# Optimization experiments

Measured on AMD Instinct MI355X. Metric: run time of the kernel, lower is better.

## Reference

```python
import jax, jax.numpy as jnp
import numpy as np

B, L, D, H, FF = 2, 2048, 2048, 16, 8192
DH = D // H
NEG = -1e9


def setup_inputs() -> dict:
    key = jax.random.key(0)
    ks = jax.random.split(key, 9)
    x = jax.random.normal(ks[0], (B, L, D), dtype=jnp.float32)
    # additive causal mask, broadcastable to [B, H, L, L]
    causal = jnp.triu(jnp.full((L, L), NEG, dtype=jnp.float32), k=1)
    mask = causal[None, None, :, :]
    s = 1.0 / np.sqrt(D)
    Wq = jax.random.normal(ks[1], (D, D), dtype=jnp.float32) * s
    Wk = jax.random.normal(ks[2], (D, D), dtype=jnp.float32) * s
    Wv = jax.random.normal(ks[3], (D, D), dtype=jnp.float32) * s
    Wo = jax.random.normal(ks[4], (D, D), dtype=jnp.float32) * s
    W_up = jax.random.normal(ks[5], (FF, D), dtype=jnp.float32) * s
    b_up = jnp.zeros((FF,), dtype=jnp.float32)
    W_down = jax.random.normal(ks[6], (D, FF), dtype=jnp.float32) * (1.0 / np.sqrt(FF))
    return {"x": x, "mask": mask, "Wq": Wq, "Wk": Wk, "Wv": Wv, "Wo": Wo,
            "W_up": W_up, "b_up": b_up, "W_down": W_down}


def reference(x, mask, Wq, Wk, Wv, Wo, W_up, b_up, W_down):
    b, l, d = x.shape
    # projections (torch Linear: y = x @ W.T); reshape to [B, H, L, DH]
    q = (x @ Wq.T).reshape(b, l, H, DH).transpose(0, 2, 1, 3)
    k = (x @ Wk.T).reshape(b, l, H, DH).transpose(0, 2, 1, 3)
    v = (x @ Wv.T).reshape(b, l, H, DH).transpose(0, 2, 1, 3)
    # NOTE: original module applies NO 1/sqrt(d_head) scaling
    scores = jnp.einsum('bhqd,bhkd->bhqk', q, k) + mask
    attn = jax.nn.softmax(scores, axis=-1)
    out = jnp.einsum('bhqk,bhkd->bhqd', attn, v)
    out = out.transpose(0, 2, 1, 3).reshape(b, l, d)
    x = x + out @ Wo.T
    h = jax.nn.relu(x @ W_up.T + b_up)
    return x + h @ W_down.T
```

## Files before the change

### kernel.cpp

```cpp
#include <hip/hip_runtime.h>
#include <stdint.h>

typedef _Float16 f16;
typedef __attribute__((ext_vector_type(8))) _Float16 f16x8;
typedef __attribute__((ext_vector_type(4))) _Float16 f16x4;
typedef __attribute__((ext_vector_type(2))) __fp16 fp16x2;
typedef __attribute__((ext_vector_type(4))) float f32x4;
typedef __attribute__((ext_vector_type(16))) float f32x16;
typedef __attribute__((ext_vector_type(4))) unsigned u32x4;

__device__ __forceinline__ void gload16(void* lds, const void* gc) {
  void* g = const_cast<void*>(gc);
  __builtin_amdgcn_global_load_lds((__attribute__((address_space(1))) void*)g,
                                   (__attribute__((address_space(3))) void*)lds,
                                   16, 0, 0);
}

__device__ __forceinline__ unsigned pkrtz(float a, float b) {
  union { fp16x2 h; unsigned u; } c;
  c.h = __builtin_amdgcn_cvt_pkrtz(a, b);
  return c.u;
}

__global__ __launch_bounds__(256) void k_cast(const float* __restrict__ in,
                                              f16* __restrict__ out, int n4) {
  int stride = gridDim.x * blockDim.x;
  for (int i = blockIdx.x * blockDim.x + threadIdx.x; i < n4; i += stride) {
    float4 v = ((const float4*)in)[i];
    f16x4 o;
    o[0] = (f16)v.x; o[1] = (f16)v.y; o[2] = (f16)v.z; o[3] = (f16)v.w;
    ((f16x4*)out)[i] = o;
  }
}

__global__ __launch_bounds__(256) void k_cast4(const float* __restrict__ s0, const float* __restrict__ s1,
                                               const float* __restrict__ s2, const float* __restrict__ s3,
                                               f16* __restrict__ d0, f16* __restrict__ d1,
                                               f16* __restrict__ d2, f16* __restrict__ d3, int n4) {
  const int which = blockIdx.y;
  const float* in = which == 0 ? s0 : which == 1 ? s1 : which == 2 ? s2 : s3;
  f16* out = which == 0 ? d0 : which == 1 ? d1 : which == 2 ? d2 : d3;
  int stride = gridDim.x * blockDim.x;
  for (int i = blockIdx.x * blockDim.x + threadIdx.x; i < n4; i += stride) {
    float4 v = ((const float4*)in)[i];
    f16x4 o;
    o[0] = (f16)v.x; o[1] = (f16)v.y; o[2] = (f16)v.z; o[3] = (f16)v.w;
    ((f16x4*)out)[i] = o;
  }
}

__global__ __launch_bounds__(256) void k_cast2w(const float* __restrict__ s0, const float* __restrict__ s1,
                                                f16* __restrict__ d0, f16* __restrict__ d1, int n4) {
  const int which = blockIdx.y;
  const float* in = which == 0 ? s0 : s1;
  f16* out = which == 0 ? d0 : d1;
  int stride = gridDim.x * blockDim.x;
  for (int i = blockIdx.x * blockDim.x + threadIdx.x; i < n4; i += stride) {
    float4 v = ((const float4*)in)[i];
    f16x4 o;
    o[0] = (f16)v.x; o[1] = (f16)v.y; o[2] = (f16)v.z; o[3] = (f16)v.w;
    ((f16x4*)out)[i] = o;
  }
}

__global__ __launch_bounds__(256) void k_transpose_v(const f16* __restrict__ vp,
                                                     f16* __restrict__ vt) {
  __shared__ __attribute__((aligned(16))) f16 tile[64][66];
  const int lt = blockIdx.x, dt = blockIdx.y, bh = blockIdx.z;
  const int t = threadIdx.x;
  const int r = t >> 3, c = 8 * (t & 7);
  const f16* src = vp + ((size_t)bh * 2048 + lt * 64) * 128 + dt * 64;
#pragma unroll
  for (int i = 0; i < 2; ++i) {
    union { f16x8 v; unsigned u[4]; } uu;
    uu.v = *(const f16x8*)&src[(size_t)(i * 32 + r) * 128 + c];
#pragma unroll
    for (int j = 0; j < 4; ++j)
      *(unsigned*)&tile[i * 32 + r][c + 2 * j] = uu.u[j];
  }
  __syncthreads();
  f16* dst = vt + ((size_t)bh * 128 + dt * 64) * 2048 + lt * 64;
#pragma unroll
  for (int i = 0; i < 2; ++i) {
    const int dr = i * 32 + r;
    f16x8 o;
#pragma unroll
    for (int e = 0; e < 8; ++e) o[e] = tile[c + e][dr];
    *(f16x8*)&dst[(size_t)dr * 2048 + c] = o;
  }
}

__global__ __launch_bounds__(256) void k_fuseout(const f16* __restrict__ x1b,
                                                 const float* __restrict__ p0,
                                                 const float* __restrict__ p1,
                                                 float* __restrict__ out, int n4) {
  int stride = gridDim.x * blockDim.x;
  for (int i = blockIdx.x * blockDim.x + threadIdx.x; i < n4; i += stride) {
    float4 a = ((const float4*)p0)[i];
    float4 b = ((const float4*)p1)[i];
    f16x4 xb = ((const f16x4*)x1b)[i];
    float4 o;
    o.x = (float)xb[0] + a.x + b.x;
    o.y = (float)xb[1] + a.y + b.y;
    o.z = (float)xb[2] + a.z + b.z;
    o.w = (float)xb[3] + a.w + b.w;
    ((float4*)out)[i] = o;
  }
}

template <int EPI, int SPLITOUT, int BK>
__global__ __launch_bounds__(256, 4) void gemm_nt(const f16* __restrict__ A,
                                                  const f16* __restrict__ B,
                                                  int Kit, int ld, int N,
                                                  const float* __restrict__ res,
                                                  f16* __restrict__ outb) {
  constexpr int TSZ = 128 * BK;
  constexpr int CH  = 2048;
  constexpr int RPC = CH / BK;
  constexpr int NCH = 128 / RPC;
  constexpr int CW  = BK / 8;
  __shared__ __attribute__((aligned(16))) f16 As[TSZ];
  __shared__ __attribute__((aligned(16))) f16 Bs[TSZ];
  const int t = threadIdx.x;
  const int l = t & 63;
  const int w = t >> 6;
  const int wr = w >> 1, wc = w & 1;

  const int nwg = gridDim.x * gridDim.y;
  const int id = blockIdx.y * gridDim.x + blockIdx.x;
  const int sw = (id & 7) * (nwg >> 3) + (id >> 3);
  const int bn = sw % gridDim.x;
  const int bm = sw / gridDim.x;

  f32x4 acc[4][4] = {};

  const size_t aoff = (size_t)bm * 128 * ld;
  const size_t boff = (size_t)bn * 128 * ld;

  const int sr = t / CW;
  const int sc = 8 * (t % CW);
  const int lbase = w * 512;

  const int lr = l & 15, lq = l >> 4;
  const int nk = Kit / BK;
  for (int kt = 0; kt < nk; ++kt) {
    const size_t gbase = (size_t)kt * BK + (size_t)sr * ld + sc;
#pragma unroll
    for (int j = 0; j < NCH; ++j) {
      gload16(As + j * CH + lbase, A + aoff + (size_t)j * RPC * ld + gbase);
      gload16(Bs + j * CH + lbase, B + boff + (size_t)j * RPC * ld + gbase);
    }
    __syncthreads();
#pragma unroll
    for (int kk = 0; kk < BK / 32; ++kk) {
      f16x8 af[4], bfr[4];
#pragma unroll
      for (int m = 0; m < 4; ++m)
        af[m] = *(const f16x8*)&As[(wr * 64 + m * 16 + lr) * BK + kk * 32 + 8 * lq];
#pragma unroll
      for (int n = 0; n < 4; ++n)
        bfr[n] = *(const f16x8*)&Bs[(wc * 64 + n * 16 + lr) * BK + kk * 32 + 8 * lq];
#pragma unroll
      for (int m = 0; m < 4; ++m)
#pragma unroll
        for (int n = 0; n < 4; ++n)
          acc[m][n] = __builtin_amdgcn_mfma_f32_16x16x32_f16(af[m], bfr[n], acc[m][n], 0, 0, 0);
    }
    __syncthreads();
  }

#pragma unroll
  for (int m = 0; m < 4; ++m) {
#pragma unroll
    for (int r = 0; r < 4; ++r) {
      const int grow = bm * 128 + wr * 64 + m * 16 + lq * 4 + r;
#pragma unroll
      for (int n = 0; n < 4; ++n) {
        const int gcol = bn * 128 + wc * 64 + n * 16 + lr;
        const size_t idx = (size_t)grow * N + gcol;
        outb[idx] = (f16)(res[idx] + acc[m][n][r]);
      }
    }
  }
}

template <int EPI, int SPLITOUT>
__global__ __launch_bounds__(512) void gemm9(const f16* __restrict__ A,
                                             const f16* __restrict__ B,
                                             int Kit, int ld, int N,
                                             const float* __restrict__ bias,
                                             float* __restrict__ outf,
                                             float* __restrict__ outf2,
                                             f16* __restrict__ outb,
                                             f16* __restrict__ outb_lo,
                                             f16* __restrict__ outv) {
  __shared__ __attribute__((aligned(16))) f16 As[32768];
  __shared__ __attribute__((aligned(16))) f16 Bs[32768];
  const int t = threadIdx.x;
  const int l = t & 63;
  const int w = t >> 6;
  const int wm = w >> 2, wn = w & 3;

  const int nwg = gridDim.x * gridDim.y;
  const int id = blockIdx.y * gridDim.x + blockIdx.x;
  const int sw = (id & 7) * (nwg >> 3) + (id >> 3);
  const int bn = sw % gridDim.x;
  const int bm = sw / gridDim.x;
  const int k0 = blockIdx.z * Kit;

  const size_t aoff = (size_t)(bm * 256) * ld + k0;
  const size_t boff = (size_t)(bn * 256) * ld + k0;

  const int r0a = t >> 3;
  const int gsw = (t & 7) ^ (r0a & 7);
  const int ldsb = (t >> 6) * 512;

  auto stageA = [&](int tile, int half) {
    const size_t col = (size_t)tile * 64 + gsw * 8;
#pragma unroll
    for (int j = 0; j < 2; ++j)
      gload16(As + (tile & 1) * 16384 + half * 8192 + j * 4096 + ldsb,
              A + aoff + (size_t)(half * 128 + j * 64 + r0a) * ld + col);
  };
  auto stageB = [&](int tile, int half) {
    const size_t col = (size_t)tile * 64 + gsw * 8;
#pragma unroll
    for (int j = 0; j < 2; ++j)
      gload16(Bs + (tile & 1) * 16384 + half * 8192 + j * 4096 + ldsb,
              B + boff + (size_t)(half * 128 + j * 64 + r0a) * ld + col);
  };

  f32x4 acc[8][4] = {};
  f16x8 af[4][2], bf[4][2];

  const int lr = l & 15, lq = l >> 4;

  auto dsA = [&](int buf, int mh) {
#pragma unroll
    for (int m = 0; m < 4; ++m) {
      const int row = mh * 64 + m * 16 + lr;
#pragma unroll
      for (int ks = 0; ks < 2; ++ks) {
        const int g = (ks * 4 + lq) ^ (row & 7);
        af[m][ks] = *(const f16x8*)&As[buf * 16384 + wm * 8192 + row * 64 + g * 8];
      }
    }
  };
  auto dsB = [&](int buf, int nh) {
#pragma unroll
    for (int n2 = 0; n2 < 2; ++n2) {
      const int row = (wn & 1) * 64 + (nh * 2 + n2) * 16 + lr;
#pragma unroll
      for (int ks = 0; ks < 2; ++ks) {
        const int g = (ks * 4 + lq) ^ (row & 7);
        bf[nh * 2 + n2][ks] = *(const f16x8*)&Bs[buf * 16384 + (wn >> 1) * 8192 + row * 64 + g * 8];
      }
    }
  };
  auto mfma16 = [&](int mh, int nh) {
    __builtin_amdgcn_s_setprio(1);
#pragma unroll
    for (int m = 0; m < 4; ++m)
#pragma unroll
      for (int n2 = 0; n2 < 2; ++n2)
#pragma unroll
        for (int ks = 0; ks < 2; ++ks)
          acc[mh * 4 + m][nh * 2 + n2] = __builtin_amdgcn_mfma_f32_16x16x32_f16(
              af[m][ks], bf[nh * 2 + n2][ks], acc[mh * 4 + m][nh * 2 + n2], 0, 0, 0);
    __builtin_amdgcn_s_setprio(0);
  };
#define BAR() __builtin_amdgcn_s_barrier()
#define LGKM() do { asm volatile("s_waitcnt lgkmcnt(0)" ::: "memory"); \
                    __builtin_amdgcn_sched_barrier(0); } while (0)

  const int ntk = Kit >> 6;
  const int nj = ntk >> 1;

  stageA(0, 0); stageA(0, 1); stageB(0, 0); stageB(0, 1);
  stageB(1, 0); stageB(1, 1);
  asm volatile("s_waitcnt vmcnt(4)" ::: "memory");
  BAR();

  for (int j = 0; j < nj; ++j) {
    const int t1 = 2 * j + 1, t2 = 2 * j + 2, t3 = 2 * j + 3;
    const bool last = (j == nj - 1);
    dsA(0, 0); dsB(0, 0);
    stageA(t1, 0);
    BAR(); LGKM(); mfma16(0, 0); BAR();
    dsB(0, 1);
    stageA(t1, 1);
    BAR(); LGKM(); mfma16(0, 1); BAR();
    dsA(0, 1);
    if (t2 < ntk) stageB(t2, 0);
    BAR(); LGKM(); mfma16(1, 0); BAR();
    if (t2 < ntk) stageB(t2, 1);
    BAR(); mfma16(1, 1);
    if (last) { asm volatile("s_waitcnt vmcnt(0)" ::: "memory"); }
    else      { asm volatile("s_waitcnt vmcnt(4)" ::: "memory"); }
    BAR();
    dsA(1, 0); dsB(1, 0);
    if (t2 < ntk) stageA(t2, 0);
    BAR(); LGKM(); mfma16(0, 0); BAR();
    dsB(1, 1);
    if (t2 < ntk) stageA(t2, 1);
    BAR(); LGKM(); mfma16(0, 1); BAR();
    dsA(1, 1);
    if (t3 < ntk) stageB(t3, 0);
    BAR(); LGKM(); mfma16(1, 0); BAR();
    if (t3 < ntk) stageB(t3, 1);
    BAR(); mfma16(1, 1);
    if (last) { asm volatile("s_waitcnt vmcnt(0)" ::: "memory"); }
    else      { asm volatile("s_waitcnt vmcnt(4)" ::: "memory"); }
    BAR();
  }
#undef BAR
#undef LGKM

  const size_t QKS = (size_t)8 << 20;
#pragma unroll
  for (int m = 0; m < 8; ++m) {
#pragma unroll
    for (int r = 0; r < 4; ++r) {
      const int grow = bm * 256 + wm * 128 + m * 16 + lq * 4 + r;
#pragma unroll
      for (int n = 0; n < 4; ++n) {
        const int gcol = bn * 256 + wn * 64 + n * 16 + lr;
        const float v = acc[m][n][r];
        if constexpr (EPI == 0) {
          const int which = gcol >> 11;
          const int hcol = gcol & 2047;
          const int bb = grow >> 11, ll = grow & 2047;
          const int hh = hcol >> 7, dh = hcol & 127;
          const size_t idx = ((size_t)((bb * 16 + hh) * 2048 + ll) << 7) + dh;
          const f16 hv = (f16)v;
          if (which == 2) {
            outv[idx] = hv;
          } else {
            outb[which * QKS + idx] = hv;
            if constexpr (SPLITOUT) outb_lo[which * QKS + idx] = (f16)(v - (float)hv);
          }
        } else if constexpr (EPI == 2) {
          const size_t idx = (size_t)grow * N + gcol;
          outb[idx] = (f16)fmaxf(v + bias[gcol], 0.f);
        } else {
          const size_t idx = (size_t)grow * N + gcol;
          (blockIdx.z ? outf2 : outf)[idx] = v;
        }
      }
    }
  }
}

__global__ __launch_bounds__(256) void k_attn(const f16* __restrict__ q_hi,
                                              const f16* __restrict__ q_lo,
                                              const f16* __restrict__ k_hi,
                                              const f16* __restrict__ k_lo,
                                              const f16* __restrict__ vtp,
                                              f16* __restrict__ op) {
  __shared__ __attribute__((aligned(16))) f16 Ks_hi[64 * 128];
  __shared__ __attribute__((aligned(16))) f16 Ks_lo[64 * 128];
  __shared__ __attribute__((aligned(16))) f16 Vs[128 * 64];
  const int t = threadIdx.x, l = t & 63, w = t >> 6;
  const int flat = (int)blockIdx.x;
  const int s_ = flat >> 5;
  const int bh = flat & 31;
  const int qb = (s_ < 8) ? (15 - s_) : (s_ - 8);
  const int q0 = qb * 128;
  const int lh = l >> 5, lm = l & 31;
  const int wrow0 = q0 + 32 * w;
  const int myrow = wrow0 + lm;

  const f16* qhp = q_hi + (size_t)bh * 2048 * 128;
  const f16* qlp = q_lo + (size_t)bh * 2048 * 128;
  const f16* khp = k_hi + (size_t)bh * 2048 * 128;
  const f16* klp = k_lo + (size_t)bh * 2048 * 128;
  const f16* vhp = vtp + (size_t)bh * 128 * 2048;

  const int krow = t >> 4, kg = t & 15;
  const int vrow = t >> 3, vg = t & 7;
  const int kgsw = kg ^ (krow & 7);
  const int vgsw = vg ^ (vrow & 7);
  const int wofs = w * 512;

  f16x8 aqh[8], aql[8];
#pragma unroll
  for (int c = 0; c < 8; ++c) {
    const size_t qi = (size_t)myrow * 128 + c * 16 + 8 * lh;
    aqh[c] = *(const f16x8*)&qhp[qi];
    aql[c] = *(const f16x8*)&qlp[qi];
  }

  f32x16 acc[4] = {};
  float mr = -1e30f, sr = 0.f;

  const int ntile = 2 * qb + 2;
  for (int kt = 0; kt < ntile; ++kt) {
    __syncthreads();
#pragma unroll
    for (int i = 0; i < 4; ++i) {
      const size_t ki = (size_t)(kt * 64 + i * 16 + krow) * 128 + 8 * kgsw;
      gload16(Ks_hi + i * 2048 + wofs, khp + ki);
      gload16(Ks_lo + i * 2048 + wofs, klp + ki);
      gload16(Vs + i * 2048 + wofs,
              vhp + (size_t)(i * 32 + vrow) * 2048 + kt * 64 + 8 * vgsw);
    }
    asm volatile("s_waitcnt vmcnt(0)" ::: "memory");
    __syncthreads();

    if (kt * 64 >= wrow0 + 32) continue;

    f32x16 s0, s1;
    __builtin_amdgcn_s_setprio(1);
    {
      f32x16 zh = {}, zl = {};
#pragma unroll
      for (int c = 0; c < 8; ++c) {
        const int g = (2 * c + lh) ^ (lm & 7);
        const f16x8 bh_ = *(const f16x8*)&Ks_hi[lm * 128 + 8 * g];
        const f16x8 bl_ = *(const f16x8*)&Ks_lo[lm * 128 + 8 * g];
        zh = __builtin_amdgcn_mfma_f32_32x32x16_f16(bh_, aqh[c], zh, 0, 0, 0);
        zl = __builtin_amdgcn_mfma_f32_32x32x16_f16(bh_, aql[c], zl, 0, 0, 0);
        zl = __builtin_amdgcn_mfma_f32_32x32x16_f16(bl_, aqh[c], zl, 0, 0, 0);
      }
      s0 = zh + zl;
    }
    {
      f32x16 zh = {}, zl = {};
#pragma unroll
      for (int c = 0; c < 8; ++c) {
        const int g = (2 * c + lh) ^ (lm & 7);
        const f16x8 bh_ = *(const f16x8*)&Ks_hi[(32 + lm) * 128 + 8 * g];
        const f16x8 bl_ = *(const f16x8*)&Ks_lo[(32 + lm) * 128 + 8 * g];
        zh = __builtin_amdgcn_mfma_f32_32x32x16_f16(bh_, aqh[c], zh, 0, 0, 0);
        zl = __builtin_amdgcn_mfma_f32_32x32x16_f16(bh_, aql[c], zl, 0, 0, 0);
        zl = __builtin_amdgcn_mfma_f32_32x32x16_f16(bl_, aqh[c], zl, 0, 0, 0);
      }
      s1 = zh + zl;
    }
    __builtin_amdgcn_s_setprio(0);

    if (kt * 64 + 63 > wrow0) {
#pragma unroll
      for (int j = 0; j < 16; ++j) {
        const int keyl = (j & 3) + 8 * (j >> 2) + 4 * lh;
        if (kt * 64 + keyl > myrow) s0[j] = -1e30f;
        if (kt * 64 + 32 + keyl > myrow) s1[j] = -1e30f;
      }
    }

    float m = -1e30f;
#pragma unroll
    for (int j = 0; j < 16; ++j) m = fmaxf(m, fmaxf(s0[j], s1[j]));
    m = fmaxf(m, __shfl_xor(m, 32));
    if (__any(m > mr + 8.f)) {
      const float mnew = fmaxf(mr, m);
      const float sc = __expf(mr - mnew);
      mr = mnew;
      sr *= sc;
#pragma unroll
      for (int j = 0; j < 16; ++j) {
        const float scj = __shfl(sc, (j & 3) + 8 * (j >> 2) + 4 * lh);
#pragma unroll
        for (int ct = 0; ct < 4; ++ct) acc[ct][j] *= scj;
      }
    }
    unsigned u[16];
    float ts = 0.f;
#pragma unroll
    for (int m2 = 0; m2 < 8; ++m2) {
      const float a0 = __expf(s0[2 * m2] - mr);
      const float a1 = __expf(s0[2 * m2 + 1] - mr);
      const float b0 = __expf(s1[2 * m2] - mr);
      const float b1 = __expf(s1[2 * m2 + 1] - mr);
      ts += (a0 + a1) + (b0 + b1);
      u[m2] = pkrtz(a0, a1);
      u[8 + m2] = pkrtz(b0, b1);
    }
    sr += ts + __shfl_xor(ts, 32);

    unsigned ys[8];
#pragma unroll
    for (int m2 = 0; m2 < 8; ++m2) {
      const int q_ = m2 >> 1, h_ = m2 & 1;
      const unsigned xs = lh ? u[4 * q_ + h_] : u[4 * q_ + 2 + h_];
      ys[m2] = __shfl_xor(xs, 32);
    }
    f16x8 pf[4];
#pragma unroll
    for (int kk = 0; kk < 4; ++kk) {
      union { u32x4 u4; f16x8 h8; } cv;
      if (lh == 0) {
        cv.u4[0] = u[4 * kk];     cv.u4[1] = u[4 * kk + 1];
        cv.u4[2] = ys[2 * kk];    cv.u4[3] = ys[2 * kk + 1];
      } else {
        cv.u4[0] = ys[2 * kk];    cv.u4[1] = ys[2 * kk + 1];
        cv.u4[2] = u[4 * kk + 2]; cv.u4[3] = u[4 * kk + 3];
      }
      pf[kk] = cv.h8;
    }

    __builtin_amdgcn_s_setprio(1);
#pragma unroll
    for (int ct = 0; ct < 4; ++ct) {
      const int dcol = ct * 32 + lm;
#pragma unroll
      for (int kk = 0; kk < 4; ++kk) {
        const int gv = (2 * kk + lh) ^ (dcol & 7);
        const f16x8 bv = *(const f16x8*)&Vs[dcol * 64 + 8 * gv];
        acc[ct] = __builtin_amdgcn_mfma_f32_32x32x16_f16(pf[kk], bv, acc[ct], 0, 0, 0);
      }
    }
    __builtin_amdgcn_s_setprio(0);
  }

  const int bb = bh >> 4, hh = bh & 15;
  const float inv = 1.f / sr;
#pragma unroll
  for (int j = 0; j < 16; ++j) {
    const int rl = (j & 3) + 8 * (j >> 2) + 4 * lh;
    const float invj = __shfl(inv, rl);
    const size_t row = (size_t)(bb * 2048 + wrow0 + rl);
#pragma unroll
    for (int ct = 0; ct < 4; ++ct)
      op[row * 2048 + hh * 128 + ct * 32 + lm] = (f16)(acc[ct][j] * invj);
  }
}

extern "C" void kernel_launch(void* const* d_in, const int* in_sizes, int n_in,
                              void* d_out, int out_size, void* d_ws, size_t ws_size,
                              hipStream_t stream) {
  const float* x   = (const float*)d_in[0];
  const float* Wq  = (const float*)d_in[2];
  const float* Wk  = (const float*)d_in[3];
  const float* Wv  = (const float*)d_in[4];
  const float* Wo  = (const float*)d_in[5];
  const float* Wup = (const float*)d_in[6];
  const float* bup = (const float*)d_in[7];
  const float* Wdn = (const float*)d_in[8];
  float* out = (float*)d_out;

  const size_t M1 = 1u << 20;
  f16* W = (f16*)d_ws;
  f16* x_hi    = W + 0 * M1;
  f16* wqkv_hi = W + 8 * M1;
  f16* wo_hi   = W + 20 * M1;
  f16* wup_hi  = W + 24 * M1;
  f16* wdn_hi  = W + 40 * M1;
  f16* q_hi    = W + 56 * M1;
  f16* q_lo    = W + 72 * M1;
  f16* vp      = W + 88 * M1;
  f16* vtb     = W + 96 * M1;
  f16* x1b   = x_hi;
  float* p0  = (float*)(W + 24 * M1);
  f16* hb    = W + 56 * M1;
  float* p1  = (float*)(W + 88 * M1);
  f16* attno = vp;
  if (ws_size < (size_t)104 * M1 * sizeof(f16)) return;

  auto cg = [](size_t n4) { size_t g = (n4 + 255) / 256; return (unsigned)(g > 2048 ? 2048 : g); };
  dim3 b256(256);
  dim3 b512(512);
  k_cast<<<cg(2 * M1), b256, 0, stream>>>(x, x_hi, (int)(2 * M1));
  k_cast4<<<dim3(cg(1 * M1), 4), b256, 0, stream>>>(
      Wq, Wk, Wv, Wo,
      wqkv_hi, wqkv_hi + 4 * M1, wqkv_hi + 8 * M1, wo_hi, (int)(1 * M1));
  k_cast2w<<<dim3(cg(4 * M1), 2), b256, 0, stream>>>(
      Wup, Wdn, wup_hi, wdn_hi, (int)(4 * M1));

  gemm9<0, 1><<<dim3(24, 16), b512, 0, stream>>>(
      x_hi, wqkv_hi, 2048, 2048, 6144,
      nullptr, nullptr, nullptr, q_hi, q_lo, vp);
  k_transpose_v<<<dim3(32, 2, 32), b256, 0, stream>>>(vp, vtb);
  k_attn<<<dim3(512), b256, 0, stream>>>(
      q_hi, q_lo, q_hi + 8 * M1, q_lo + 8 * M1, vtb, attno);
  gemm_nt<1, 0, 64><<<dim3(16, 32), b256, 0, stream>>>(
      attno, wo_hi, 2048, 2048, 2048, x, x1b);
  gemm9<2, 0><<<dim3(32, 16), b512, 0, stream>>>(
      x1b, wup_hi, 2048, 2048, 8192,
      bup, nullptr, nullptr, hb, nullptr, nullptr);
  gemm9<3, 0><<<dim3(8, 16, 2), b512, 0, stream>>>(
      hb, wdn_hi, 4096, 8192, 2048,
      nullptr, p0, p1, nullptr, nullptr, nullptr);
  k_fuseout<<<2048, b256, 0, stream>>>(x1b, p0, p1, out, (int)(2 * M1));
}
```

Baseline: 697.3 us.

## Double-buffer K tiles and overlap global loads with attention compute

Restructures the attention loop so the next K tile (hi and lo) is prefetched into a second LDS buffer while the current QK^T and softmax run. V staging is moved to the end of each iteration, and vmcnt waits are scoped so only the needed loads block. This is meant to hide global-to-LDS latency that previously stalled every iteration, at the cost of doubled K LDS usage, which may reduce occupancy, and extra barriers per iteration.

```diff
diff --git a/kernel.cpp b/kernel.cpp
--- a/kernel.cpp
+++ b/kernel.cpp
@@ -357,9 +357,9 @@
                                               const f16* __restrict__ k_lo,
                                               const f16* __restrict__ vtp,
                                               f16* __restrict__ op) {
-  __shared__ __attribute__((aligned(16))) f16 Ks_hi[64 * 128];
-  __shared__ __attribute__((aligned(16))) f16 Ks_lo[64 * 128];
-  __shared__ __attribute__((aligned(16))) f16 Vs[128 * 64];
+  __shared__ __attribute__((aligned(16))) f16 Ks_hi[2 * 8192];
+  __shared__ __attribute__((aligned(16))) f16 Ks_lo[2 * 8192];
+  __shared__ __attribute__((aligned(16))) f16 Vs[8192];
   const int t = threadIdx.x, l = t & 63, w = t >> 6;
   const int flat = (int)blockIdx.x;
   const int s_ = flat >> 5;
@@ -382,6 +382,21 @@
   const int vgsw = vg ^ (vrow & 7);
   const int wofs = w * 512;
 
+  auto stageK = [&](int tile, int kb) {
+#pragma unroll
+    for (int i = 0; i < 4; ++i) {
+      const size_t ki = (size_t)(tile * 64 + i * 16 + krow) * 128 + 8 * kgsw;
+      gload16(Ks_hi + kb * 8192 + i * 2048 + wofs, khp + ki);
+      gload16(Ks_lo + kb * 8192 + i * 2048 + wofs, klp + ki);
+    }
+  };
+  auto stageV = [&](int tile) {
+#pragma unroll
+    for (int i = 0; i < 4; ++i)
+      gload16(Vs + i * 2048 + wofs,
+              vhp + (size_t)(i * 32 + vrow) * 2048 + tile * 64 + 8 * vgsw);
+  };
+
   f16x8 aqh[8], aql[8];
 #pragma unroll
   for (int c = 0; c < 8; ++c) {
@@ -394,124 +409,137 @@
   float mr = -1e30f, sr = 0.f;
 
   const int ntile = 2 * qb + 2;
+  stageK(0, 0);
+  stageV(0);
+  asm volatile("s_waitcnt vmcnt(0)" ::: "memory");
+  __syncthreads();
+
   for (int kt = 0; kt < ntile; ++kt) {
-    __syncthreads();
-#pragma unroll
-    for (int i = 0; i < 4; ++i) {
-      const size_t ki = (size_t)(kt * 64 + i * 16 + krow) * 128 + 8 * kgsw;
-      gload16(Ks_hi + i * 2048 + wofs, khp + ki);
-      gload16(Ks_lo + i * 2048 + wofs, klp + ki);
-      gload16(Vs + i * 2048 + wofs,
-              vhp + (size_t)(i * 32 + vrow) * 2048 + kt * 64 + 8 * vgsw);
-    }
-    asm volatile("s_waitcnt vmcnt(0)" ::: "memory");
-    __syncthreads();
-
-    if (kt * 64 >= wrow0 + 32) continue;
+    const int kb = kt & 1;
+    const bool active = (kt * 64 < wrow0 + 32);
+    const int tn = (kt + 1 < ntile) ? (kt + 1) : (ntile - 1);
 
     f32x16 s0, s1;
-    __builtin_amdgcn_s_setprio(1);
-    {
-      f32x16 zh = {}, zl = {};
-#pragma unroll
-      for (int c = 0; c < 8; ++c) {
-        const int g = (2 * c + lh) ^ (lm & 7);
-        const f16x8 bh_ = *(const f16x8*)&Ks_hi[lm * 128 + 8 * g];
-        const f16x8 bl_ = *(const f16x8*)&Ks_lo[lm * 128 + 8 * g];
-        zh = __builtin_amdgcn_mfma_f32_32x32x16_f16(bh_, aqh[c], zh, 0, 0, 0);
-        zl = __builtin_amdgcn_mfma_f32_32x32x16_f16(bh_, aql[c], zl, 0, 0, 0);
-        zl = __builtin_amdgcn_mfma_f32_32x32x16_f16(bl_, aqh[c], zl, 0, 0, 0);
-      }
-      s0 = zh + zl;
-    }
-    {
-      f32x16 zh = {}, zl = {};
-#pragma unroll
-      for (int c = 0; c < 8; ++c) {
-        const int g = (2 * c + lh) ^ (lm & 7);
-        const f16x8 bh_ = *(const f16x8*)&Ks_hi[(32 + lm) * 128 + 8 * g];
-        const f16x8 bl_ = *(const f16x8*)&Ks_lo[(32 + lm) * 128 + 8 * g];
-        zh = __builtin_amdgcn_mfma_f32_32x32x16_f16(bh_, aqh[c], zh, 0, 0, 0);
-        zl = __builtin_amdgcn_mfma_f32_32x32x16_f16(bh_, aql[c], zl, 0, 0, 0);
-        zl = __builtin_amdgcn_mfma_f32_32x32x16_f16(bl_, aqh[c], zl, 0, 0, 0);
-      }
-      s1 = zh + zl;
-    }
-    __builtin_amdgcn_s_setprio(0);
-
-    if (kt * 64 + 63 > wrow0) {
-#pragma unroll
-      for (int j = 0; j < 16; ++j) {
-        const int keyl = (j & 3) + 8 * (j >> 2) + 4 * lh;
-        if (kt * 64 + keyl > myrow) s0[j] = -1e30f;
-        if (kt * 64 + 32 + keyl > myrow) s1[j] = -1e30f;
-      }
-    }
-
-    float m = -1e30f;
-#pragma unroll
-    for (int j = 0; j < 16; ++j) m = fmaxf(m, fmaxf(s0[j], s1[j]));
-    m = fmaxf(m, __shfl_xor(m, 32));
-    if (__any(m > mr + 8.f)) {
-      const float mnew = fmaxf(mr, m);
-      const float sc = __expf(mr - mnew);
-      mr = mnew;
-      sr *= sc;
-#pragma unroll
-      for (int j = 0; j < 16; ++j) {
-        const float scj = __shfl(sc, (j & 3) + 8 * (j >> 2) + 4 * lh);
-#pragma unroll
-        for (int ct = 0; ct < 4; ++ct) acc[ct][j] *= scj;
-      }
-    }
     unsigned u[16];
     float ts = 0.f;
-#pragma unroll
-    for (int m2 = 0; m2 < 8; ++m2) {
-      const float a0 = __expf(s0[2 * m2] - mr);
-      const float a1 = __expf(s0[2 * m2 + 1] - mr);
-      const float b0 = __expf(s1[2 * m2] - mr);
-      const float b1 = __expf(s1[2 * m2 + 1] - mr);
-      ts += (a0 + a1) + (b0 + b1);
-      u[m2] = pkrtz(a0, a1);
-      u[8 + m2] = pkrtz(b0, b1);
-    }
-    sr += ts + __shfl_xor(ts, 32);
-
-    unsigned ys[8];
-#pragma unroll
-    for (int m2 = 0; m2 < 8; ++m2) {
-      const int q_ = m2 >> 1, h_ = m2 & 1;
-      const unsigned xs = lh ? u[4 * q_ + h_] : u[4 * q_ + 2 + h_];
-      ys[m2] = __shfl_xor(xs, 32);
-    }
-    f16x8 pf[4];
-#pragma unroll
-    for (int kk = 0; kk < 4; ++kk) {
-      union { u32x4 u4; f16x8 h8; } cv;
-      if (lh == 0) {
-        cv.u4[0] = u[4 * kk];     cv.u4[1] = u[4 * kk + 1];
-        cv.u4[2] = ys[2 * kk];    cv.u4[3] = ys[2 * kk + 1];
-      } else {
-        cv.u4[0] = ys[2 * kk];    cv.u4[1] = ys[2 * kk + 1];
-        cv.u4[2] = u[4 * kk + 2]; cv.u4[3] = u[4 * kk + 3];
-      }
-      pf[kk] = cv.h8;
-    }
-
-    __builtin_amdgcn_s_setprio(1);
-#pragma unroll
-    for (int ct = 0; ct < 4; ++ct) {
-      const int dcol = ct * 32 + lm;
+
+    if (active) {
+      const f16* Kh = Ks_hi + kb * 8192;
+      const f16* Kl = Ks_lo + kb * 8192;
+      __builtin_amdgcn_s_setprio(1);
+      {
+        f32x16 zh = {}, zl = {};
+#pragma unroll
+        for (int c = 0; c < 8; ++c) {
+          const int g = (2 * c + lh) ^ (lm & 7);
+          const f16x8 bh_ = *(const f16x8*)&Kh[lm * 128 + 8 * g];
+          const f16x8 bl_ = *(const f16x8*)&Kl[lm * 128 + 8 * g];
+          zh = __builtin_amdgcn_mfma_f32_32x32x16_f16(bh_, aqh[c], zh, 0, 0, 0);
+          zl = __builtin_amdgcn_mfma_f32_32x32x16_f16(bh_, aql[c], zl, 0, 0, 0);
+          zl = __builtin_amdgcn_mfma_f32_32x32x16_f16(bl_, aqh[c], zl, 0, 0, 0);
+        }
+        s0 = zh + zl;
+      }
+      {
+        f32x16 zh = {}, zl = {};
+#pragma unroll
+        for (int c = 0; c < 8; ++c) {
+          const int g = (2 * c + lh) ^ (lm & 7);
+          const f16x8 bh_ = *(const f16x8*)&Kh[(32 + lm) * 128 + 8 * g];
+          const f16x8 bl_ = *(const f16x8*)&Kl[(32 + lm) * 128 + 8 * g];
+          zh = __builtin_amdgcn_mfma_f32_32x32x16_f16(bh_, aqh[c], zh, 0, 0, 0);
+          zl = __builtin_amdgcn_mfma_f32_32x32x16_f16(bh_, aql[c], zl, 0, 0, 0);
+          zl = __builtin_amdgcn_mfma_f32_32x32x16_f16(bl_, aqh[c], zl, 0, 0, 0);
+        }
+        s1 = zh + zl;
+      }
+      __builtin_amdgcn_s_setprio(0);
+    }
+
+    stageK(tn, kb ^ 1);
+
+    if (active) {
+      if (kt * 64 + 63 > wrow0) {
+#pragma unroll
+        for (int j = 0; j < 16; ++j) {
+          const int keyl = (j & 3) + 8 * (j >> 2) + 4 * lh;
+          if (kt * 64 + keyl > myrow) s0[j] = -1e30f;
+          if (kt * 64 + 32 + keyl > myrow) s1[j] = -1e30f;
+        }
+      }
+      float m = -1e30f;
+#pragma unroll
+      for (int j = 0; j < 16; ++j) m = fmaxf(m, fmaxf(s0[j], s1[j]));
+      m = fmaxf(m, __shfl_xor(m, 32));
+      if (__any(m > mr + 8.f)) {
+        const float mnew = fmaxf(mr, m);
+        const float sc = __expf(mr - mnew);
+        mr = mnew;
+        sr *= sc;
+#pragma unroll
+        for (int j = 0; j < 16; ++j) {
+          const float scj = __shfl(sc, (j & 3) + 8 * (j >> 2) + 4 * lh);
+#pragma unroll
+          for (int ct = 0; ct < 4; ++ct) acc[ct][j] *= scj;
+        }
+      }
+#pragma unroll
+      for (int m2 = 0; m2 < 8; ++m2) {
+        const float a0 = __expf(s0[2 * m2] - mr);
+        const float a1 = __expf(s0[2 * m2 + 1] - mr);
+        const float b0 = __expf(s1[2 * m2] - mr);
+        const float b1 = __expf(s1[2 * m2 + 1] - mr);
+        ts += (a0 + a1) + (b0 + b1);
+        u[m2] = pkrtz(a0, a1);
+        u[8 + m2] = pkrtz(b0, b1);
+      }
+      sr += ts + __shfl_xor(ts, 32);
+    }
+
+    asm volatile("s_waitcnt vmcnt(8)" ::: "memory");
+    __syncthreads();
+
+    if (active) {
+      unsigned ys[8];
+#pragma unroll
+      for (int m2 = 0; m2 < 8; ++m2) {
+        const int q_ = m2 >> 1, h_ = m2 & 1;
+        const unsigned xs = lh ? u[4 * q_ + h_] : u[4 * q_ + 2 + h_];
+        ys[m2] = __shfl_xor(xs, 32);
+      }
+      f16x8 pf[4];
 #pragma unroll
       for (int kk = 0; kk < 4; ++kk) {
-        const int gv = (2 * kk + lh) ^ (dcol & 7);
-        const f16x8 bv = *(const f16x8*)&Vs[dcol * 64 + 8 * gv];
-        acc[ct] = __builtin_amdgcn_mfma_f32_32x32x16_f16(pf[kk], bv, acc[ct], 0, 0, 0);
-      }
-    }
-    __builtin_amdgcn_s_setprio(0);
-  }
+        union { u32x4 u4; f16x8 h8; } cv;
+        if (lh == 0) {
+          cv.u4[0] = u[4 * kk];     cv.u4[1] = u[4 * kk + 1];
+          cv.u4[2] = ys[2 * kk];    cv.u4[3] = ys[2 * kk + 1];
+        } else {
+          cv.u4[0] = ys[2 * kk];    cv.u4[1] = ys[2 * kk + 1];
+          cv.u4[2] = u[4 * kk + 2]; cv.u4[3] = u[4 * kk + 3];
+        }
+        pf[kk] = cv.h8;
+      }
+      __builtin_amdgcn_s_setprio(1);
+#pragma unroll
+      for (int ct = 0; ct < 4; ++ct) {
+        const int dcol = ct * 32 + lm;
+#pragma unroll
+        for (int kk = 0; kk < 4; ++kk) {
+          const int gv = (2 * kk + lh) ^ (dcol & 7);
+          const f16x8 bv = *(const f16x8*)&Vs[dcol * 64 + 8 * gv];
+          acc[ct] = __builtin_amdgcn_mfma_f32_32x32x16_f16(pf[kk], bv, acc[ct], 0, 0, 0);
+        }
+      }
+      __builtin_amdgcn_s_setprio(0);
+    }
+
+    __syncthreads();
+    stageV(tn);
+    asm volatile("s_waitcnt vmcnt(4)" ::: "memory");
+    __syncthreads();
+  }
+  asm volatile("s_waitcnt vmcnt(0)" ::: "memory");
 
   const int bb = bh >> 4, hh = bh & 15;
   const float inv = 1.f / sr;
```

Measured after the change: 702.7 us. About the same (+0.8%).
